# Performance work log

Measured on AMD Instinct MI355X. Metric: run time of the kernel, lower is better.

Reference implementation:

```python
import jax, jax.numpy as jnp
import numpy as np
from jax import lax

K_NBR = 9  # K nearest neighbors
R = 2      # shuffle_scale


def pixel_unshuffle(x, r):
    B, C, H, W = x.shape
    x = x.reshape(B, C, H // r, r, W // r, r)
    return x.transpose(0, 1, 3, 5, 2, 4).reshape(B, C * r * r, H // r, W // r)


def pixel_shuffle(x, r):
    B, C, H, W = x.shape
    x = x.reshape(B, C // (r * r), r, r, H, W)
    return x.transpose(0, 1, 4, 2, 5, 3).reshape(B, C // (r * r), H * r, W * r)


def conv2d_same(x, w, b):
    y = lax.conv_general_dilated(x, w, (1, 1), 'SAME',
                                 dimension_numbers=('NCHW', 'OIHW', 'NCHW'))
    return y + b[None, :, None, None]


def convnn_branching_layer(x, idx, wa, ba, wb, bb, wp, bp):
    """Conv2d_ConvNN_Random_Branching with shuffle_pattern='BA'."""
    x = pixel_unshuffle(x, R)                      # (B, C*r^2, H/r, W/r)
    B, C, H, W = x.shape
    T = H * W
    # Branch 1: standard 3x3 conv
    y1 = conv2d_same(x, wa, ba)                    # (B, c1, H, W)
    # Branch 2: ConvNN on K nearest of N random samples
    xt = x.reshape(B, C, T)                        # tokens
    samp = xt[:, :, idx]                           # (B, C, N) random samples
    dots = jnp.einsum('bct,bcn->btn', xt, samp)
    xn = jnp.sum(xt * xt, axis=1)[:, :, None]      # (B, T, 1)
    sn = jnp.sum(samp * samp, axis=1)[:, None, :]  # (B, 1, N)
    dist = xn + sn - 2.0 * dots                    # squared euclidean (B, T, N)
    nbr = lax.top_k(-dist, K_NBR)[1]               # (B, T, K) indices into samples
    # gather neighbor features: (B, C, T*K)
    g = jnp.take_along_axis(samp, nbr.reshape(B, 1, T * K_NBR), axis=2)
    g = g.reshape(B, C, T, K_NBR)
    # Conv1d(kernel=K, stride=K) over stacked neighbors
    y2 = jnp.einsum('bctk,ock->bot', g, wb) + bb[None, :, None]
    y2 = y2.reshape(B, wb.shape[0], H, W)          # (B, c2, H, W)
    y = jax.nn.relu(jnp.concatenate([y1, y2], axis=1))
    y = conv2d_same(y, wp, bp)                     # 1x1 -> out*r^2 channels
    return pixel_shuffle(y, R)                     # (B, out, H*r, W*r)


def setup_inputs() -> dict:
    key = jax.random.key(0)
    ks = jax.random.split(key, 24)
    s = 0.02
    B = 256
    inp = {
        'x': jax.random.normal(ks[0], (B, 3, 32, 32), jnp.float32),
        'idx1': jax.random.randint(ks[1], (64,), 0, 256, jnp.int32),
        'idx2': jax.random.randint(ks[2], (64,), 0, 256, jnp.int32),
        # layer 1: Cin = 3*4 = 12, branches 16+16, out 16*4 = 64 pre-shuffle
        'w1a': jax.random.normal(ks[3], (16, 12, 3, 3), jnp.float32) * s,
        'b1a': jnp.zeros((16,), jnp.float32),
        'w1b': jax.random.normal(ks[4], (16, 12, 9), jnp.float32) * s,
        'b1b': jnp.zeros((16,), jnp.float32),
        'w1p': jax.random.normal(ks[5], (64, 32, 1, 1), jnp.float32) * s,
        'b1p': jnp.zeros((64,), jnp.float32),
        # layer 2: Cin = 16*4 = 64, branches 32+32, out 32*4 = 128 pre-shuffle
        'w2a': jax.random.normal(ks[6], (32, 64, 3, 3), jnp.float32) * s,
        'b2a': jnp.zeros((32,), jnp.float32),
        'w2b': jax.random.normal(ks[7], (32, 64, 9), jnp.float32) * s,
        'b2b': jnp.zeros((32,), jnp.float32),
        'w2p': jax.random.normal(ks[8], (128, 64, 1, 1), jnp.float32) * s,
        'b2p': jnp.zeros((128,), jnp.float32),
        # FC head
        'fc1w': jax.random.normal(ks[9], (1024, 32768), jnp.float32) * s,
        'fc1b': jnp.zeros((1024,), jnp.float32),
        'fc2w': jax.random.normal(ks[10], (10, 1024), jnp.float32) * s,
        'fc2b': jnp.zeros((10,), jnp.float32),
    }
    return inp


def reference(x, idx1, idx2, w1a, b1a, w1b, b1b, w1p, b1p,
              w2a, b2a, w2b, b2b, w2p, b2p, fc1w, fc1b, fc2w, fc2b):
    h = convnn_branching_layer(x, idx1, w1a, b1a, w1b, b1b, w1p, b1p)  # (B,16,32,32)
    h = convnn_branching_layer(h, idx2, w2a, b2a, w2b, b2b, w2p, b2p)  # (B,32,32,32)
    h = h.reshape(h.shape[0], -1)                   # (B, 32768)
    h = jax.nn.relu(h @ fc1w.T + fc1b)
    return h @ fc2w.T + fc2b                        # (B, num_classes)
```

## Files before the change

kernel.cpp:

```cpp
#include <hip/hip_runtime.h>
#include <cstdint>
#include <cstddef>


#define DI static __device__ __forceinline__

typedef __attribute__((ext_vector_type(8))) short short8;
typedef __attribute__((ext_vector_type(4))) float f32x4;

DI unsigned short f2bf(float v) {
  unsigned u = __builtin_bit_cast(unsigned, v);
  unsigned r = (u + 0x7FFFu + ((u >> 16) & 1u)) >> 16;
  return (unsigned short)r;
}
DI float bf2f(unsigned short h) {
  unsigned u = ((unsigned)h) << 16;
  return __builtin_bit_cast(float, u);
}

DI float xu1_at(const float* __restrict__ x, int b, int c, int t) {
  int h = t >> 4, w = t & 15;
  return x[(((size_t)b * 3 + (c >> 2)) * 32 + 2 * h + ((c >> 1) & 1)) * 32 + 2 * w + (c & 1)];
}

__global__ __launch_bounds__(256) void k_prepw(
    const float* __restrict__ w1b, float* __restrict__ wT1,
    const float* __restrict__ w2b, float* __restrict__ wT2,
    const float* __restrict__ w1p, float* __restrict__ wp1T,
    const float* __restrict__ w2p, float* __restrict__ wp2T,
    const float* __restrict__ w1a, float* __restrict__ wa1T,
    const float* __restrict__ w2a, float* __restrict__ wa2T)
{
  int i = blockIdx.x * 256 + threadIdx.x;
  if (i < 1728) {
    int k = i / 192, r = i % 192, c = r >> 4, o = r & 15;
    wT1[i] = w1b[((size_t)o * 12 + c) * 9 + k];
    return;
  }
  i -= 1728;
  if (i < 18432) {
    int k = i / 2048, r = i % 2048, c = r >> 5, o = r & 31;
    wT2[i] = w2b[((size_t)o * 64 + c) * 9 + k];
    return;
  }
  i -= 18432;
  if (i < 2048) { int ic = i >> 6, o = i & 63; wp1T[i] = w1p[(size_t)o * 32 + ic]; return; }
  i -= 2048;
  if (i < 8192) { int ic = i >> 7, o = i & 127; wp2T[i] = w2p[(size_t)o * 64 + ic]; return; }
  i -= 8192;
  if (i < 1728) {
    int o = i & 15, u = i >> 4, ic = u / 9, tp = u % 9;
    wa1T[i] = w1a[((size_t)o * 12 + ic) * 9 + tp];
    return;
  }
  i -= 1728;
  if (i < 18432) {
    int o = i & 31, u = i >> 5, ic = u / 9, tp = u % 9;
    wa2T[i] = w2a[((size_t)o * 64 + ic) * 9 + tp];
  }
}

template <int CIN, bool GATHER, int CCTOT, int OCT>
__global__ __launch_bounds__(256) void k_conv3x3(
    const float* __restrict__ xsrc, const float* __restrict__ xu,
    const float* __restrict__ waT, const float* __restrict__ bias,
    float* __restrict__ ycat)
{
  int b = blockIdx.x;
  int ocb = blockIdx.y * 16;
  __shared__ float xs[CIN * 256];
  int t = threadIdx.x;
  if (GATHER) {
    for (int i = t; i < CIN * 256; i += 256) {
      int c = i >> 8, tt = i & 255;
      xs[i] = xu1_at(xsrc, b, c, tt);
    }
  } else {
    for (int i = t; i < CIN * 256; i += 256) xs[i] = xu[(size_t)b * CIN * 256 + i];
  }
  __syncthreads();
  int tt = t & 127, og = t >> 7;
  int oc0 = ocb + og * 8;
  int h0 = tt >> 4, wc = tt & 15;
  float acc0[8], acc1[8];
#pragma unroll
  for (int o = 0; o < 8; ++o) { acc0[o] = bias[oc0 + o]; acc1[o] = acc0[o]; }
  bool vw0 = wc > 0, vw2 = wc < 15, vh0 = h0 > 0, vh7 = h0 < 7;
  bool m0v[9] = {vh0 && vw0, vh0, vh0 && vw2, vw0, true, vw2, vw0, true, vw2};
  bool m1v[9] = {vw0, true, vw2, vw0, true, vw2, vh7 && vw0, vh7, vh7 && vw2};
  int tc0[9], tc1[9];
#pragma unroll
  for (int dh = 0; dh < 3; ++dh)
#pragma unroll
    for (int dw = 0; dw < 3; ++dw) {
      int o0 = (h0 + dh - 1) * 16 + (wc + dw - 1);
      int o1 = (h0 + 8 + dh - 1) * 16 + (wc + dw - 1);
      tc0[dh * 3 + dw] = o0 < 0 ? 0 : (o0 > 255 ? 255 : o0);
      tc1[dh * 3 + dw] = o1 < 0 ? 0 : (o1 > 255 ? 255 : o1);
    }
#pragma unroll 2
  for (int ic = 0; ic < CIN; ++ic) {
    float xv0[9], xv1[9];
#pragma unroll
    for (int tp = 0; tp < 9; ++tp) {
      float v0 = xs[ic * 256 + tc0[tp]];
      float v1 = xs[ic * 256 + tc1[tp]];
      xv0[tp] = m0v[tp] ? v0 : 0.f;
      xv1[tp] = m1v[tp] ? v1 : 0.f;
    }
#pragma unroll
    for (int tp = 0; tp < 9; ++tp) {
      const float* wp = waT + ((size_t)ic * 9 + tp) * OCT + oc0;
      float4 wA = *(const float4*)wp;
      float4 wB = *(const float4*)(wp + 4);
      float wv[8] = {wA.x, wA.y, wA.z, wA.w, wB.x, wB.y, wB.z, wB.w};
#pragma unroll
      for (int o = 0; o < 8; ++o) {
        acc0[o] = fmaf(xv0[tp], wv[o], acc0[o]);
        acc1[o] = fmaf(xv1[tp], wv[o], acc1[o]);
      }
    }
  }
#pragma unroll
  for (int o = 0; o < 8; ++o) {
    ycat[((size_t)b * CCTOT + oc0 + o) * 256 + tt] = fmaxf(acc0[o], 0.f);
    ycat[((size_t)b * CCTOT + oc0 + o) * 256 + tt + 128] = fmaxf(acc1[o], 0.f);
  }
}

template <int C, int STR, bool GATHER>
__global__ __launch_bounds__(256) void k_prep(
    const float* __restrict__ xsrc, const float* __restrict__ xu,
    const int* __restrict__ idx,
    float* __restrict__ sampT, float* __restrict__ samp_cn,
    float* __restrict__ snvg)
{
  int b = blockIdx.x, t = threadIdx.x;
  __shared__ float sph[C * 64];
  __shared__ int idxs[64];
  if (t < 64) idxs[t] = idx[t];
  __syncthreads();
  for (int i = t; i < C * 64; i += 256) {
    int c = i >> 6, n = i & 63;
    int p = idxs[n];
    sph[i] = GATHER ? xu1_at(xsrc, b, c, p) : xu[((size_t)b * C + c) * 256 + p];
  }
  __syncthreads();
  for (int i = t; i < C * 64; i += 256) samp_cn[(size_t)b * C * 64 + i] = sph[i];
  for (int i = t; i < 64 * STR; i += 256) {
    int n = i / STR, c = i % STR;
    if (c < C) sampT[(size_t)b * 64 * STR + i] = sph[c * 64 + n];
  }
  if (t < 64) {
    float s;
    {
#pragma clang fp contract(off)
      s = 0.f;
      for (int c = 0; c < C; ++c) { float v = sph[c * 64 + t]; s += v * v; }
    }
    snvg[(size_t)b * 64 + t] = s;
  }
}

template <int C, int STR, bool GATHER>
__global__ __launch_bounds__(256) void k_nbr(
    const float* __restrict__ xsrc, const float* __restrict__ xu,
    const float* __restrict__ sampT, const float* __restrict__ snvg,
    int* __restrict__ nbr)
{
  int b = blockIdx.x, t = threadIdx.x;
  float xcol[C];
#pragma unroll
  for (int c = 0; c < C; ++c)
    xcol[c] = GATHER ? xu1_at(xsrc, b, c, t) : xu[((size_t)b * C + c) * 256 + t];
  float xn;
  {
#pragma clang fp contract(off)
    xn = 0.f;
#pragma unroll
    for (int c = 0; c < C; ++c) xn += xcol[c] * xcol[c];
  }
  float bd[9];
  int bn[9];
#pragma unroll
  for (int i = 0; i < 9; ++i) { bd[i] = __builtin_inff(); bn[i] = 1 << 30; }

#pragma unroll 1
  for (int n = 0; n < 64; ++n) {
    const float* sp = sampT + ((size_t)b * 64 + n) * STR;
    float snvn = snvg[(size_t)b * 64 + n];
    float d;
    {
#pragma clang fp contract(off)
      float dot = 0.f;
#pragma unroll
      for (int c = 0; c < C; ++c) dot = fmaf(xcol[c], sp[c], dot);
      d = (xn + snvn) - 2.f * dot;
    }
    if (d < bd[8] || (d == bd[8] && n < bn[8])) {
      float dc = d;
      int nc = n;
#pragma unroll
      for (int i = 0; i < 9; ++i) {
        bool sw = (dc < bd[i]) || (dc == bd[i] && nc < bn[i]);
        float ob = bd[i]; int on = bn[i];
        bd[i] = sw ? dc : ob; bn[i] = sw ? nc : on;
        dc = sw ? ob : dc;   nc = sw ? on : nc;
      }
    }
  }
#pragma unroll
  for (int k = 0; k < 9; ++k) nbr[((size_t)b * 9 + k) * 256 + t] = bn[k];
}

template <int C, int OPT, int OTOT, int CCTOT, int OCBASE>
__global__ __launch_bounds__(256) void k_einsum(
    const float* __restrict__ samp_cn,
    const int* __restrict__ nbr,
    const float* __restrict__ wT,
    const float* __restrict__ bb,
    float* __restrict__ ycat)
{
  int b = blockIdx.x, t = threadIdx.x;
  int tt = t & 127, og = t >> 7;
  int o0 = og * OPT;
  __shared__ float samps[C * 64];
  for (int i = t; i < C * 64; i += 256)
    samps[i] = samp_cn[(size_t)b * C * 64 + i];
  int bnA[9], bnB[9];
#pragma unroll
  for (int k = 0; k < 9; ++k) {
    bnA[k] = nbr[((size_t)b * 9 + k) * 256 + tt];
    bnB[k] = nbr[((size_t)b * 9 + k) * 256 + tt + 128];
  }
  __syncthreads();
  float acc0[OPT], acc1[OPT];
#pragma unroll
  for (int o = 0; o < OPT; ++o) { acc0[o] = bb[o0 + o]; acc1[o] = acc0[o]; }
#pragma unroll 1
  for (int k = 0; k < 9; ++k) {
    int n0 = bnA[k], n1 = bnB[k];
#pragma unroll 2
    for (int c = 0; c < C; ++c) {
      float sv0 = samps[c * 64 + n0];
      float sv1 = samps[c * 64 + n1];
      const float* wp = wT + ((size_t)k * C + c) * OTOT + o0;
#pragma unroll
      for (int oq = 0; oq < OPT / 4; ++oq) {
        float4 wv = ((const float4*)wp)[oq];
        float w4[4] = {wv.x, wv.y, wv.z, wv.w};
#pragma unroll
        for (int j = 0; j < 4; ++j) {
          acc0[oq * 4 + j] = fmaf(sv0, w4[j], acc0[oq * 4 + j]);
          acc1[oq * 4 + j] = fmaf(sv1, w4[j], acc1[oq * 4 + j]);
        }
      }
    }
  }
#pragma unroll
  for (int o = 0; o < OPT; ++o) {
    ycat[((size_t)b * CCTOT + OCBASE + o0 + o) * 256 + tt] = fmaxf(acc0[o], 0.f);
    ycat[((size_t)b * CCTOT + OCBASE + o0 + o) * 256 + tt + 128] = fmaxf(acc1[o], 0.f);
  }
}

template <int CIN, int OPT, int OCTOT, bool SHUF>
__global__ __launch_bounds__(256) void k_conv1x1(
    const float* __restrict__ yin, const float* __restrict__ wpT,
    const float* __restrict__ bias, float* __restrict__ out)
{
  int b = blockIdx.x, ocb = blockIdx.y * 2 * OPT, t = threadIdx.x;
  int tt = t & 127, og = t >> 7;
  int o0 = ocb + og * OPT;
  __shared__ float ys[CIN * 256];
  for (int i = t; i < CIN * 256; i += 256) ys[i] = yin[(size_t)b * CIN * 256 + i];
  __syncthreads();
  float acc0[OPT], acc1[OPT];
#pragma unroll
  for (int o = 0; o < OPT; ++o) { acc0[o] = bias[o0 + o]; acc1[o] = acc0[o]; }
#pragma unroll 2
  for (int ic = 0; ic < CIN; ++ic) {
    float sv0 = ys[ic * 256 + tt];
    float sv1 = ys[ic * 256 + tt + 128];
    const float* wp = wpT + (size_t)ic * OCTOT + o0;
#pragma unroll
    for (int oq = 0; oq < OPT / 4; ++oq) {
      float4 wv = ((const float4*)wp)[oq];
      float w4[4] = {wv.x, wv.y, wv.z, wv.w};
#pragma unroll
      for (int j = 0; j < 4; ++j) {
        acc0[oq * 4 + j] = fmaf(sv0, w4[j], acc0[oq * 4 + j]);
        acc1[oq * 4 + j] = fmaf(sv1, w4[j], acc1[oq * 4 + j]);
      }
    }
  }
  int h0 = tt >> 4, wc = tt & 15;
#pragma unroll
  for (int o = 0; o < OPT; ++o) {
    int ogl = o0 + o;
    if (SHUF) {
      int f0 = (ogl >> 2) * 1024 + (2 * h0 + ((ogl >> 1) & 1)) * 32 + (2 * wc + (ogl & 1));
      int f1 = (ogl >> 2) * 1024 + (2 * (h0 + 8) + ((ogl >> 1) & 1)) * 32 + (2 * wc + (ogl & 1));
      out[(size_t)b * 32768 + f0] = acc0[o];
      out[(size_t)b * 32768 + f1] = acc1[o];
    } else {
      out[((size_t)b * OCTOT + ogl) * 256 + tt] = acc0[o];
      out[((size_t)b * OCTOT + ogl) * 256 + tt + 128] = acc1[o];
    }
  }
}

__global__ __launch_bounds__(256, 3) void k_fc1(
    const float* __restrict__ A, const float* __restrict__ W,
    float* __restrict__ parts)
{
  constexpr int KTOT = 32768;
  constexpr int LDT = 40;
  __shared__ unsigned short Ah[64 * LDT], Am[64 * LDT], Al[64 * LDT];
  int t = threadIdx.x;
  int nb = blockIdx.x, mb = blockIdx.y, sb = blockIdx.z;
  int m0 = mb * 64, n0 = nb * 128, k0 = sb * 1024;
  int wave = t >> 6, lane = t & 63;
  int q = lane >> 4, m16 = lane & 15;

  f32x4 acc[4][2];
#pragma unroll
  for (int mt = 0; mt < 4; ++mt)
#pragma unroll
    for (int nt = 0; nt < 2; ++nt) acc[mt][nt] = (f32x4){0.f, 0.f, 0.f, 0.f};

  int r8 = t >> 3, c4 = t & 7;
  const float* A0 = A + (size_t)(m0 + r8) * KTOT + k0 + c4 * 4;
  const float* A1 = A + (size_t)(m0 + r8 + 32) * KTOT + k0 + c4 * 4;
  const float* W0 = W + (size_t)(n0 + wave * 32 + m16) * KTOT + k0 + q * 8;
  const float* W1 = W + (size_t)(n0 + wave * 32 + 16 + m16) * KTOT + k0 + q * 8;

  for (int ks = 0; ks < 1024; ks += 32) {
    float4 a0 = *(const float4*)(A0 + ks);
    float4 a1 = *(const float4*)(A1 + ks);
    float4 w0a = *(const float4*)(W0 + ks), w0b = *(const float4*)(W0 + ks + 4);
    float4 w1a = *(const float4*)(W1 + ks), w1b = *(const float4*)(W1 + ks + 4);
    __syncthreads();
    {
      float vv[8] = {a0.x, a0.y, a0.z, a0.w, a1.x, a1.y, a1.z, a1.w};
      int off0 = r8 * LDT + c4 * 4, off1 = (r8 + 32) * LDT + c4 * 4;
      ushort4 h4, m4, l4;
#pragma unroll
      for (int g = 0; g < 2; ++g) {
        {
          float v = vv[g * 4 + 0]; h4.x = f2bf(v); float r1 = v - bf2f(h4.x);
          m4.x = f2bf(r1); l4.x = f2bf(r1 - bf2f(m4.x));
        }
        {
          float v = vv[g * 4 + 1]; h4.y = f2bf(v); float r1 = v - bf2f(h4.y);
          m4.y = f2bf(r1); l4.y = f2bf(r1 - bf2f(m4.y));
        }
        {
          float v = vv[g * 4 + 2]; h4.z = f2bf(v); float r1 = v - bf2f(h4.z);
          m4.z = f2bf(r1); l4.z = f2bf(r1 - bf2f(m4.z));
        }
        {
          float v = vv[g * 4 + 3]; h4.w = f2bf(v); float r1 = v - bf2f(h4.w);
          m4.w = f2bf(r1); l4.w = f2bf(r1 - bf2f(m4.w));
        }
        int off = g == 0 ? off0 : off1;
        *(ushort4*)&Ah[off] = h4; *(ushort4*)&Am[off] = m4; *(ushort4*)&Al[off] = l4;
      }
    }
    __syncthreads();
    short8 bh[2], bm[2], bl[2];
    {
      float wf0[8] = {w0a.x, w0a.y, w0a.z, w0a.w, w0b.x, w0b.y, w0b.z, w0b.w};
      float wf1[8] = {w1a.x, w1a.y, w1a.z, w1a.w, w1b.x, w1b.y, w1b.z, w1b.w};
#pragma unroll
      for (int j = 0; j < 8; ++j) {
        unsigned short h = f2bf(wf0[j]); float r1 = wf0[j] - bf2f(h);
        unsigned short m = f2bf(r1);
        bh[0][j] = (short)h; bm[0][j] = (short)m; bl[0][j] = (short)f2bf(r1 - bf2f(m));
        h = f2bf(wf1[j]); r1 = wf1[j] - bf2f(h);
        m = f2bf(r1);
        bh[1][j] = (short)h; bm[1][j] = (short)m; bl[1][j] = (short)f2bf(r1 - bf2f(m));
      }
    }
#pragma unroll
    for (int mt = 0; mt < 4; ++mt) {
      int aoff = (mt * 16 + m16) * LDT + q * 8;
      short8 ah = *(const short8*)&Ah[aoff];
      short8 am = *(const short8*)&Am[aoff];
      short8 al = *(const short8*)&Al[aoff];
#pragma unroll
      for (int nt = 0; nt < 2; ++nt) {
        acc[mt][nt] = __builtin_amdgcn_mfma_f32_16x16x32_bf16(al, bh[nt], acc[mt][nt], 0, 0, 0);
        acc[mt][nt] = __builtin_amdgcn_mfma_f32_16x16x32_bf16(am, bm[nt], acc[mt][nt], 0, 0, 0);
        acc[mt][nt] = __builtin_amdgcn_mfma_f32_16x16x32_bf16(ah, bl[nt], acc[mt][nt], 0, 0, 0);
        acc[mt][nt] = __builtin_amdgcn_mfma_f32_16x16x32_bf16(am, bh[nt], acc[mt][nt], 0, 0, 0);
        acc[mt][nt] = __builtin_amdgcn_mfma_f32_16x16x32_bf16(ah, bm[nt], acc[mt][nt], 0, 0, 0);
        acc[mt][nt] = __builtin_amdgcn_mfma_f32_16x16x32_bf16(ah, bh[nt], acc[mt][nt], 0, 0, 0);
      }
    }
  }
  float* P = parts + (size_t)sb * 262144;
#pragma unroll
  for (int mt = 0; mt < 4; ++mt)
#pragma unroll
    for (int nt = 0; nt < 2; ++nt)
#pragma unroll
      for (int r2 = 0; r2 < 4; ++r2) {
        int m = m0 + mt * 16 + q * 4 + r2;
        int n = n0 + wave * 32 + nt * 16 + m16;
        P[(size_t)m * 1024 + n] = acc[mt][nt][r2];
      }
}

__global__ __launch_bounds__(256) void k_fc1_reduce(const float* __restrict__ parts,
                                                    const float* __restrict__ bias,
                                                    float* __restrict__ h1) {
  int i = blockIdx.x * 256 + threadIdx.x;
  float s = 0.f;
#pragma unroll
  for (int sb = 0; sb < 32; ++sb) s += parts[(size_t)sb * 262144 + i];
  h1[i] = fmaxf(s + bias[i & 1023], 0.f);
}

__global__ __launch_bounds__(256) void k_fc2(const float* __restrict__ h1,
                                             const float* __restrict__ w,
                                             const float* __restrict__ bias,
                                             float* __restrict__ out)
{
  int m = blockIdx.x, tid = threadIdx.x;
  __shared__ float hs[1024];
  __shared__ float ps[256];
  for (int i = tid; i < 1024; i += 256) hs[i] = h1[(size_t)m * 1024 + i];
  __syncthreads();
  int n = tid >> 4, sl = tid & 15;
  float p = 0.f;
  if (n < 10) {
    const float* wr = w + (size_t)n * 1024 + sl * 64;
    const float* hr = hs + sl * 64;
#pragma unroll 8
    for (int j = 0; j < 64; ++j) p = fmaf(hr[j], wr[j], p);
  }
  ps[tid] = p;
  __syncthreads();
  if (sl == 0 && n < 10) {
    float s = 0.f;
#pragma unroll
    for (int q = 0; q < 16; ++q) s += ps[n * 16 + q];
    out[(size_t)m * 10 + n] = s + bias[n];
  }
}

extern "C" void kernel_launch(void* const* d_in, const int* in_sizes, int n_in,
                              void* d_out, int out_size, void* d_ws, size_t ws_size,
                              hipStream_t stream) {
  (void)in_sizes; (void)n_in; (void)out_size; (void)ws_size;
  const float* x    = (const float*)d_in[0];
  const int*   idx1 = (const int*)d_in[1];
  const int*   idx2 = (const int*)d_in[2];
  const float* w1a  = (const float*)d_in[3];
  const float* b1a  = (const float*)d_in[4];
  const float* w1b  = (const float*)d_in[5];
  const float* b1b  = (const float*)d_in[6];
  const float* w1p  = (const float*)d_in[7];
  const float* b1p  = (const float*)d_in[8];
  const float* w2a  = (const float*)d_in[9];
  const float* b2a  = (const float*)d_in[10];
  const float* w2b  = (const float*)d_in[11];
  const float* b2b  = (const float*)d_in[12];
  const float* w2p  = (const float*)d_in[13];
  const float* b2p  = (const float*)d_in[14];
  const float* fc1w = (const float*)d_in[15];
  const float* fc1b = (const float*)d_in[16];
  const float* fc2w = (const float*)d_in[17];
  const float* fc2b = (const float*)d_in[18];

  float* ws    = (float*)d_ws;
  float* xu2   = ws + 0;
  float* ycat1 = ws + 4194304;
  float* ycat2 = ws + 4194304;
  float* WGT   = ws + 8388608;
  float* wT1   = WGT + 0;
  float* wT2   = WGT + 1728;
  float* wp1T  = WGT + 20160;
  float* wp2T  = WGT + 22208;
  float* wa1T  = WGT + 30400;
  float* wa2T  = WGT + 32128;
  float* h1    = ws + 8650752;
  float* hshuf = ws + 10485760;
  float* H        = ws + 10485760;
  int*   nbr      = (int*)(H + 0);
  float* sampT1   = H + 589824;
  float* snv1     = H + 851968;
  float* sampT2   = H + 868352;
  float* snv2     = H + 1916928;
  float* samp_cn1 = H + 1933312;
  float* samp_cn2 = H + 2129920;
  float* parts = ws + 0;
  float* out   = (float*)d_out;

  k_prepw<<<198, 256, 0, stream>>>(w1b, wT1, w2b, wT2, w1p, wp1T, w2p, wp2T, w1a, wa1T, w2a, wa2T);
  k_conv3x3<12, true, 32, 16><<<dim3(256, 1), 256, 0, stream>>>(x, nullptr, wa1T, b1a, ycat1);
  k_prep<12, 16, true><<<256, 256, 0, stream>>>(x, nullptr, idx1, sampT1, samp_cn1, snv1);
  k_nbr<12, 16, true><<<256, 256, 0, stream>>>(x, nullptr, sampT1, snv1, nbr);
  k_einsum<12, 8, 16, 32, 16><<<256, 256, 0, stream>>>(samp_cn1, nbr, wT1, b1b, ycat1);
  k_conv1x1<32, 32, 64, false><<<dim3(256, 1), 256, 0, stream>>>(ycat1, wp1T, b1p, xu2);
  k_conv3x3<64, false, 64, 32><<<dim3(256, 2), 256, 0, stream>>>(nullptr, xu2, wa2T, b2a, ycat2);
  k_prep<64, 64, false><<<256, 256, 0, stream>>>(nullptr, xu2, idx2, sampT2, samp_cn2, snv2);
  k_nbr<64, 64, false><<<256, 256, 0, stream>>>(nullptr, xu2, sampT2, snv2, nbr);
  k_einsum<64, 16, 32, 64, 32><<<256, 256, 0, stream>>>(samp_cn2, nbr, wT2, b2b, ycat2);
  k_conv1x1<64, 32, 128, true><<<dim3(256, 2), 256, 0, stream>>>(ycat2, wp2T, b2p, hshuf);
  k_fc1<<<dim3(8, 4, 32), 256, 0, stream>>>(hshuf, fc1w, parts);
  k_fc1_reduce<<<1024, 256, 0, stream>>>(parts, fc1b, h1);
  k_fc2<<<256, 256, 0, stream>>>(h1, fc2w, fc2b, out);
}
```

Measured before the change: 696.7 us.

## Double M tile of fc1 GEMM and register-prefetch next K slice

The fc1 split-K GEMM block tile grows from 64 to 128 rows of the activation matrix. Each weight fragment, along with its three-way bf16 split, is now reused across twice as many MFMAs, and the grid shrinks from 1024 to 512 blocks. The global loads for the next K step are issued into registers before the current step's conversion and MFMA work, so memory latency overlaps compute. The cost is a doubled accumulator array and larger LDS use, which lowers occupancy (launch bounds drop from 3 to 2 blocks per CU). The final iteration also issues a wasted reload of the first K slice.

```diff
diff --git a/kernel.cpp b/kernel.cpp
--- a/kernel.cpp
+++ b/kernel.cpp
@@ -310,64 +310,46 @@
   }
 }
 
-__global__ __launch_bounds__(256, 3) void k_fc1(
+__global__ __launch_bounds__(256, 2) void k_fc1(
     const float* __restrict__ A, const float* __restrict__ W,
     float* __restrict__ parts)
 {
   constexpr int KTOT = 32768;
   constexpr int LDT = 40;
-  __shared__ unsigned short Ah[64 * LDT], Am[64 * LDT], Al[64 * LDT];
+  __shared__ unsigned short Ah[128 * LDT], Am[128 * LDT], Al[128 * LDT];
   int t = threadIdx.x;
   int nb = blockIdx.x, mb = blockIdx.y, sb = blockIdx.z;
-  int m0 = mb * 64, n0 = nb * 128, k0 = sb * 1024;
+  int m0 = mb * 128, n0 = nb * 128, k0 = sb * 1024;
   int wave = t >> 6, lane = t & 63;
   int q = lane >> 4, m16 = lane & 15;
 
-  f32x4 acc[4][2];
-#pragma unroll
-  for (int mt = 0; mt < 4; ++mt)
+  f32x4 acc[8][2];
+#pragma unroll
+  for (int mt = 0; mt < 8; ++mt)
 #pragma unroll
     for (int nt = 0; nt < 2; ++nt) acc[mt][nt] = (f32x4){0.f, 0.f, 0.f, 0.f};
 
-  int r8 = t >> 3, c4 = t & 7;
-  const float* A0 = A + (size_t)(m0 + r8) * KTOT + k0 + c4 * 4;
-  const float* A1 = A + (size_t)(m0 + r8 + 32) * KTOT + k0 + c4 * 4;
+  int arow = t >> 1, acol = (t & 1) * 16;
+  const float* Ap = A + (size_t)(m0 + arow) * KTOT + k0 + acol;
   const float* W0 = W + (size_t)(n0 + wave * 32 + m16) * KTOT + k0 + q * 8;
   const float* W1 = W + (size_t)(n0 + wave * 32 + 16 + m16) * KTOT + k0 + q * 8;
 
+  float4 aR0 = *(const float4*)(Ap + 0);
+  float4 aR1 = *(const float4*)(Ap + 4);
+  float4 aR2 = *(const float4*)(Ap + 8);
+  float4 aR3 = *(const float4*)(Ap + 12);
+  float4 w0a = *(const float4*)(W0), w0b = *(const float4*)(W0 + 4);
+  float4 w1a = *(const float4*)(W1), w1b = *(const float4*)(W1 + 4);
+
   for (int ks = 0; ks < 1024; ks += 32) {
-    float4 a0 = *(const float4*)(A0 + ks);
-    float4 a1 = *(const float4*)(A1 + ks);
-    float4 w0a = *(const float4*)(W0 + ks), w0b = *(const float4*)(W0 + ks + 4);
-    float4 w1a = *(const float4*)(W1 + ks), w1b = *(const float4*)(W1 + ks + 4);
-    __syncthreads();
-    {
-      float vv[8] = {a0.x, a0.y, a0.z, a0.w, a1.x, a1.y, a1.z, a1.w};
-      int off0 = r8 * LDT + c4 * 4, off1 = (r8 + 32) * LDT + c4 * 4;
-      ushort4 h4, m4, l4;
-#pragma unroll
-      for (int g = 0; g < 2; ++g) {
-        {
-          float v = vv[g * 4 + 0]; h4.x = f2bf(v); float r1 = v - bf2f(h4.x);
-          m4.x = f2bf(r1); l4.x = f2bf(r1 - bf2f(m4.x));
-        }
-        {
-          float v = vv[g * 4 + 1]; h4.y = f2bf(v); float r1 = v - bf2f(h4.y);
-          m4.y = f2bf(r1); l4.y = f2bf(r1 - bf2f(m4.y));
-        }
-        {
-          float v = vv[g * 4 + 2]; h4.z = f2bf(v); float r1 = v - bf2f(h4.z);
-          m4.z = f2bf(r1); l4.z = f2bf(r1 - bf2f(m4.z));
-        }
-        {
-          float v = vv[g * 4 + 3]; h4.w = f2bf(v); float r1 = v - bf2f(h4.w);
-          m4.w = f2bf(r1); l4.w = f2bf(r1 - bf2f(m4.w));
-        }
-        int off = g == 0 ? off0 : off1;
-        *(ushort4*)&Ah[off] = h4; *(ushort4*)&Am[off] = m4; *(ushort4*)&Al[off] = l4;
-      }
-    }
-    __syncthreads();
+    int ksn = (ks + 32 < 1024) ? ks + 32 : 0;
+    float4 nA0 = *(const float4*)(Ap + ksn);
+    float4 nA1 = *(const float4*)(Ap + ksn + 4);
+    float4 nA2 = *(const float4*)(Ap + ksn + 8);
+    float4 nA3 = *(const float4*)(Ap + ksn + 12);
+    float4 nW0a = *(const float4*)(W0 + ksn), nW0b = *(const float4*)(W0 + ksn + 4);
+    float4 nW1a = *(const float4*)(W1 + ksn), nW1b = *(const float4*)(W1 + ksn + 4);
+
     short8 bh[2], bm[2], bl[2];
     {
       float wf0[8] = {w0a.x, w0a.y, w0a.z, w0a.w, w0b.x, w0b.y, w0b.z, w0b.w};
@@ -382,8 +364,36 @@
         bh[1][j] = (short)h; bm[1][j] = (short)m; bl[1][j] = (short)f2bf(r1 - bf2f(m));
       }
     }
-#pragma unroll
-    for (int mt = 0; mt < 4; ++mt) {
+    short8 vh0, vh1, vm0, vm1, vl0, vl1;
+    {
+      float av[16] = {aR0.x, aR0.y, aR0.z, aR0.w, aR1.x, aR1.y, aR1.z, aR1.w,
+                      aR2.x, aR2.y, aR2.z, aR2.w, aR3.x, aR3.y, aR3.z, aR3.w};
+#pragma unroll
+      for (int j = 0; j < 8; ++j) {
+        {
+          float v = av[j];
+          unsigned short h = f2bf(v); float r1 = v - bf2f(h);
+          unsigned short m = f2bf(r1);
+          vh0[j] = (short)h; vm0[j] = (short)m; vl0[j] = (short)f2bf(r1 - bf2f(m));
+        }
+        {
+          float v = av[j + 8];
+          unsigned short h = f2bf(v); float r1 = v - bf2f(h);
+          unsigned short m = f2bf(r1);
+          vh1[j] = (short)h; vm1[j] = (short)m; vl1[j] = (short)f2bf(r1 - bf2f(m));
+        }
+      }
+    }
+    __syncthreads();
+    {
+      int off = arow * LDT + acol;
+      *(short8*)&Ah[off] = vh0; *(short8*)&Ah[off + 8] = vh1;
+      *(short8*)&Am[off] = vm0; *(short8*)&Am[off + 8] = vm1;
+      *(short8*)&Al[off] = vl0; *(short8*)&Al[off + 8] = vl1;
+    }
+    __syncthreads();
+#pragma unroll
+    for (int mt = 0; mt < 8; ++mt) {
       int aoff = (mt * 16 + m16) * LDT + q * 8;
       short8 ah = *(const short8*)&Ah[aoff];
       short8 am = *(const short8*)&Am[aoff];
@@ -398,10 +408,12 @@
         acc[mt][nt] = __builtin_amdgcn_mfma_f32_16x16x32_bf16(ah, bh[nt], acc[mt][nt], 0, 0, 0);
       }
     }
+    aR0 = nA0; aR1 = nA1; aR2 = nA2; aR3 = nA3;
+    w0a = nW0a; w0b = nW0b; w1a = nW1a; w1b = nW1b;
   }
   float* P = parts + (size_t)sb * 262144;
 #pragma unroll
-  for (int mt = 0; mt < 4; ++mt)
+  for (int mt = 0; mt < 8; ++mt)
 #pragma unroll
     for (int nt = 0; nt < 2; ++nt)
 #pragma unroll
@@ -509,7 +521,7 @@
   k_nbr<64, 64, false><<<256, 256, 0, stream>>>(nullptr, xu2, sampT2, snv2, nbr);
   k_einsum<64, 16, 32, 64, 32><<<256, 256, 0, stream>>>(samp_cn2, nbr, wT2, b2b, ycat2);
   k_conv1x1<64, 32, 128, true><<<dim3(256, 2), 256, 0, stream>>>(ycat2, wp2T, b2p, hshuf);
-  k_fc1<<<dim3(8, 4, 32), 256, 0, stream>>>(hshuf, fc1w, parts);
+  k_fc1<<<dim3(8, 2, 32), 256, 0, stream>>>(hshuf, fc1w, parts);
   k_fc1_reduce<<<1024, 256, 0, stream>>>(parts, fc1b, h1);
   k_fc2<<<256, 256, 0, stream>>>(h1, fc2w, fc2b, out);
 }
```

Result: no change. 686.1 us (-1.5%).
